# Kernel tuning notes

Measured on AMD Instinct MI355X. Metric: run time of the kernel, lower is better.

The kernel has to match this reference:

```python
import jax, jax.numpy as jnp
import numpy as np

N, IN_C, OUT_C, FEAT_C, G = 1_000_000, 64, 64, 128, 4096


def setup_inputs() -> dict:
    key = jax.random.key(0)
    ks = jax.random.split(key, 9)
    x = jax.random.normal(ks[0], (N, IN_C), dtype=jnp.float32)
    origin_feat = jax.random.normal(ks[1], (G, FEAT_C), dtype=jnp.float32)
    latent_point_batch = jax.random.randint(ks[2], (N,), 0, G, dtype=jnp.int32)
    s_fc = 1.0 / np.sqrt(IN_C)
    s_ft = 1.0 / np.sqrt(FEAT_C)
    W_fc = jax.random.uniform(ks[3], (IN_C, OUT_C), jnp.float32, -s_fc, s_fc)
    b_fc = jax.random.uniform(ks[4], (OUT_C,), jnp.float32, -s_fc, s_fc)
    W_mu = jax.random.uniform(ks[5], (FEAT_C, OUT_C), jnp.float32, -s_ft, s_ft)
    b_mu = jax.random.uniform(ks[6], (OUT_C,), jnp.float32, -s_ft, s_ft)
    W_sig = jax.random.uniform(ks[7], (FEAT_C, OUT_C), jnp.float32, -s_ft, s_ft)
    b_sig = jax.random.uniform(ks[8], (OUT_C,), jnp.float32, -s_ft, s_ft)
    return {"x": x, "origin_feat": origin_feat, "latent_point_batch": latent_point_batch,
            "num_groups": G, "W_fc": W_fc, "b_fc": b_fc, "W_mu": W_mu, "b_mu": b_mu,
            "W_sig": W_sig, "b_sig": b_sig}


def _segment_mean(v, seg, num_segments):
    # [N, C] -> [G, C] per-segment mean
    s = jax.ops.segment_sum(v, seg, num_segments=num_segments)
    cnt = jax.ops.segment_sum(jnp.ones((v.shape[0],), v.dtype), seg,
                              num_segments=num_segments)
    return s / jnp.maximum(cnt, 1.0)[:, None]


def reference(x, origin_feat, latent_point_batch, num_groups,
              W_fc, b_fc, W_mu, b_mu, W_sig, b_sig):
    h = x @ W_fc + b_fc                      # [N, outC]
    mu = origin_feat @ W_mu + b_mu           # [G, outC]
    sig = origin_feat @ W_sig + b_sig        # [G, outC]
    seg = latent_point_batch
    h_mean = _segment_mean(h, seg, num_groups)          # [G, outC]
    h_c = h - h_mean[seg]                                # centered
    h_var = _segment_mean(h_c * h_c, seg, num_groups)    # biased var per group
    h_n = h_c / jnp.sqrt(h_var[seg] + 1e-14)
    out = jax.nn.relu(h_n * sig[seg] + mu[seg])
    return out
```

## Files before the change

### kernel.cpp

```cpp
#include <hip/hip_runtime.h>
#include <stdint.h>

#define GMAX 4096
#define NB   256
#define CH   64

__global__ void FCAdaINLayer_68719477052_kernel(int* __restrict__ cnt, int G) {
  int t = blockIdx.x * blockDim.x + threadIdx.x;
  int stride = gridDim.x * blockDim.x;
  for (int i = t; i < G; i += stride) cnt[i] = 0;
}

__global__ __launch_bounds__(256) void k_bhist(const int* __restrict__ lat, int n, int G,
                                               int* __restrict__ hist_b) {
  __shared__ int h[GMAX];
  int b = blockIdx.x, t = threadIdx.x;
  for (int g = t; g < G; g += 256) h[g] = 0;
  __syncthreads();
  int chb = (n + NB - 1) / NB;
  int beg = b * chb, end = min(beg + chb, n);
  for (int i = beg + t; i < end; i += 256) atomicAdd(&h[lat[i]], 1);
  __syncthreads();
  for (int g = t; g < G; g += 256) hist_b[(size_t)b * G + g] = h[g];
}

__global__ void k_scanA(int* __restrict__ hist_b, int G, int* __restrict__ cnt) {
  int g = blockIdx.x * blockDim.x + threadIdx.x;
  if (g >= G) return;
  int run = 0;
  for (int b = 0; b < NB; b++) {
    int v = hist_b[(size_t)b * G + g];
    hist_b[(size_t)b * G + g] = run;
    run += v;
  }
  cnt[g] = run;
}

__global__ void k_scanB(const int* __restrict__ cnt, int G, int* __restrict__ offs) {
  __shared__ int part[256];
  int t = threadIdx.x;
  int per = (G + 255) / 256;
  int base = t * per;
  int s = 0;
  for (int j = 0; j < per; j++) { int g = base + j; if (g < G) s += cnt[g]; }
  part[t] = s;
  __syncthreads();
  if (t == 0) {
    int run = 0;
    for (int j = 0; j < 256; j++) { int v = part[j]; part[j] = run; run += v; }
  }
  __syncthreads();
  int run = part[t];
  for (int j = 0; j < per; j++) {
    int g = base + j;
    if (g < G) { offs[g] = run; run += cnt[g]; }
  }
  if (t == 255) offs[G] = run;
}

__global__ __launch_bounds__(256) void k_scatter2(const int* __restrict__ lat, int n, int G,
                                                  const int* __restrict__ offs,
                                                  const int* __restrict__ hist_b,
                                                  int* __restrict__ sorted) {
  __shared__ int cur[GMAX];
  int b = blockIdx.x, t = threadIdx.x;
  for (int g = t; g < G; g += 256) cur[g] = offs[g] + hist_b[(size_t)b * G + g];
  __syncthreads();
  int chb = (n + NB - 1) / NB;
  int beg = b * chb, end = min(beg + chb, n);
  for (int i = beg + t; i < end; i += 256) {
    int g = lat[i];
    int pos = atomicAdd(&cur[g], 1);
    sorted[pos] = i;
  }
}

__device__ __forceinline__ float dot64(const float4* __restrict__ xr,
                                       const float* wcol, float bc) {
  float h0 = bc, h1 = 0.f, h2 = 0.f, h3 = 0.f;
#pragma unroll
  for (int j = 0; j < 16; j++) {
    float4 q = xr[j];
    int k = j * 4;
    h0 = fmaf(q.x, wcol[k], h0);
    h1 = fmaf(q.y, wcol[k + 1], h1);
    h2 = fmaf(q.z, wcol[k + 2], h2);
    h3 = fmaf(q.w, wcol[k + 3], h3);
  }
  return (h0 + h2) + (h1 + h3);
}

__global__ __launch_bounds__(256) void k_stats(
    const float* __restrict__ x, const int* __restrict__ sorted,
    const int* __restrict__ offs, const float* __restrict__ of,
    const float* __restrict__ Wmu, const float* __restrict__ bmu,
    const float* __restrict__ Wsig, const float* __restrict__ bsig,
    const float* __restrict__ Wfc, const float* __restrict__ bfc,
    float* __restrict__ scaleT, float* __restrict__ shiftT) {
  __shared__ float xs[CH * 64];
  __shared__ float red[2][4][64];
  int g = blockIdx.x;
  int beg = offs[g], end = offs[g + 1];
  int cnt = end - beg;
  if (cnt == 0) return;
  int tid = threadIdx.x, lane = tid & 63, wid = tid >> 6;

  float wcol[64];
#pragma unroll
  for (int k = 0; k < 64; k++) wcol[k] = Wfc[k * 64 + lane];
  float bc = bfc[lane];

  float ssum = 0.f, ssq = 0.f;
  for (int c0 = 0; c0 < cnt; c0 += CH) {
    int rows = min(CH, cnt - c0);
    __syncthreads();
    for (int idx = tid; idx < rows * 16; idx += 256) {
      int j = idx >> 4, e = idx & 15;
      int p = sorted[beg + c0 + j];
      reinterpret_cast<float4*>(xs)[j * 16 + e] =
          reinterpret_cast<const float4*>(x + (size_t)p * 64)[e];
    }
    __syncthreads();
    for (int j = wid; j < rows; j += 4) {
      float h = dot64(reinterpret_cast<const float4*>(xs + j * 64), wcol, bc);
      ssum += h;
      ssq = fmaf(h, h, ssq);
    }
  }
  red[0][wid][lane] = ssum;
  red[1][wid][lane] = ssq;
  __syncthreads();
  if (wid == 0) {
    float ts = 0.f, tq = 0.f;
#pragma unroll
    for (int w = 0; w < 4; w++) { ts += red[0][w][lane]; tq += red[1][w][lane]; }
    float inv = 1.0f / (float)cnt;
    float mean = ts * inv;
    float var = fmaxf(tq * inv - mean * mean, 0.f);
    float rstd = rsqrtf(var + 1e-14f);
    const float* ofr = of + (size_t)g * 128;
    float a0 = 0.f, a1 = 0.f;
    for (int k = 0; k < 128; k++) {
      float ov = ofr[k];
      a0 = fmaf(ov, Wmu[k * 64 + lane], a0);
      a1 = fmaf(ov, Wsig[k * 64 + lane], a1);
    }
    float mu = a0 + bmu[lane];
    float sig = a1 + bsig[lane];
    float sc = sig * rstd;
    scaleT[(size_t)g * 64 + lane] = sc;
    shiftT[(size_t)g * 64 + lane] = mu - mean * sc;
  }
}

__global__ __launch_bounds__(256) void k_applyn(
    const float* __restrict__ x, const int* __restrict__ lat, int n,
    const float* __restrict__ scaleT, const float* __restrict__ shiftT,
    const float* __restrict__ Wfc, const float* __restrict__ bfc,
    float* __restrict__ out) {
  __shared__ float xs[CH * 64];
  int tid = threadIdx.x, lane = tid & 63, wid = tid >> 6;
  float wcol[64];
#pragma unroll
  for (int k = 0; k < 64; k++) wcol[k] = Wfc[k * 64 + lane];
  float bc = bfc[lane];

  int nchunks = (n + CH - 1) / CH;
  for (int c = blockIdx.x; c < nchunks; c += gridDim.x) {
    int p0 = c * CH;
    int rows = min(CH, n - p0);
    __syncthreads();
    for (int idx = tid; idx < rows * 16; idx += 256) {
      reinterpret_cast<float4*>(xs)[idx] =
          reinterpret_cast<const float4*>(x + (size_t)p0 * 64)[idx];
    }
    __syncthreads();
    for (int j = wid; j < rows; j += 4) {
      int p = p0 + j;
      int g = lat[p];
      float h = dot64(reinterpret_cast<const float4*>(xs + j * 64), wcol, bc);
      float sc = scaleT[(size_t)g * 64 + lane];
      float sh = shiftT[(size_t)g * 64 + lane];
      out[(size_t)p * 64 + lane] = fmaxf(fmaf(h, sc, sh), 0.f);
    }
  }
}

extern "C" void kernel_launch(void* const* d_in, const int* in_sizes, int n_in,
                              void* d_out, int out_size, void* d_ws, size_t ws_size,
                              hipStream_t stream) {
  const float* x   = (const float*)d_in[0];
  const float* of  = (const float*)d_in[1];
  const int* lat   = (const int*)d_in[2];
  const float* Wfc = (const float*)d_in[4];
  const float* bfc = (const float*)d_in[5];
  const float* Wmu = (const float*)d_in[6];
  const float* bmu = (const float*)d_in[7];
  const float* Wsg = (const float*)d_in[8];
  const float* bsg = (const float*)d_in[9];

  int N = in_sizes[2];
  int G = in_sizes[1] / 128;

  char* ws = (char*)d_ws;
  size_t o = 0;
  int* cnt     = (int*)(ws + o); o += (size_t)G * 4;
  int* offs    = (int*)(ws + o); o += (size_t)(G + 1) * 4;
  o = (o + 255) & ~(size_t)255;
  int* hist_b  = (int*)(ws + o); o += (size_t)NB * G * 4;
  int* sorted  = (int*)(ws + o); o += (size_t)N * 4;
  float* scT   = (float*)(ws + o); o += (size_t)G * 64 * 4;
  float* shT   = (float*)(ws + o); o += (size_t)G * 64 * 4;

  FCAdaINLayer_68719477052_kernel<<<32, 256, 0, stream>>>(cnt, G);
  k_bhist<<<NB, 256, 0, stream>>>(lat, N, G, hist_b);
  k_scanA<<<(G + 255) / 256, 256, 0, stream>>>(hist_b, G, cnt);
  k_scanB<<<1, 256, 0, stream>>>(cnt, G, offs);
  k_scatter2<<<NB, 256, 0, stream>>>(lat, N, G, offs, hist_b, sorted);
  k_stats<<<G, 256, 0, stream>>>(x, sorted, offs, of, Wmu, bmu, Wsg, bsg, Wfc, bfc, scT, shT);
  k_applyn<<<2048, 256, 0, stream>>>(x, lat, N, scT, shT, Wfc, bfc, (float*)d_out);
}
```

Before: 925.1 us.

## Read x rows directly via wave-uniform scalar loads instead of LDS staging

Both the stats and apply kernels stop staging x rows through shared memory with block-wide barriers. Each wave now reads its rows straight from global memory, using readfirstlane so the row address is wave-uniform and the loads can become scalar/broadcast loads, and handles two rows per iteration for more memory-level parallelism. This removes the LDS copy and the __syncthreads overhead, at the cost of relying on the scalar cache path and losing the coalesced bulk loads.

Measured after the change: 1.129 ms. 22.1% more time.

```diff
diff --git a/kernel.cpp b/kernel.cpp
--- a/kernel.cpp
+++ b/kernel.cpp
@@ -3,7 +3,6 @@
 
 #define GMAX 4096
 #define NB   256
-#define CH   64
 
 __global__ void FCAdaINLayer_68719477052_kernel(int* __restrict__ cnt, int G) {
   int t = blockIdx.x * blockDim.x + threadIdx.x;
@@ -97,7 +96,6 @@
     const float* __restrict__ Wsig, const float* __restrict__ bsig,
     const float* __restrict__ Wfc, const float* __restrict__ bfc,
     float* __restrict__ scaleT, float* __restrict__ shiftT) {
-  __shared__ float xs[CH * 64];
   __shared__ float red[2][4][64];
   int g = blockIdx.x;
   int beg = offs[g], end = offs[g + 1];
@@ -111,20 +109,18 @@
   float bc = bfc[lane];
 
   float ssum = 0.f, ssq = 0.f;
-  for (int c0 = 0; c0 < cnt; c0 += CH) {
-    int rows = min(CH, cnt - c0);
-    __syncthreads();
-    for (int idx = tid; idx < rows * 16; idx += 256) {
-      int j = idx >> 4, e = idx & 15;
-      int p = sorted[beg + c0 + j];
-      reinterpret_cast<float4*>(xs)[j * 16 + e] =
-          reinterpret_cast<const float4*>(x + (size_t)p * 64)[e];
-    }
-    __syncthreads();
-    for (int j = wid; j < rows; j += 4) {
-      float h = dot64(reinterpret_cast<const float4*>(xs + j * 64), wcol, bc);
-      ssum += h;
-      ssq = fmaf(h, h, ssq);
+  for (int j = wid; j < cnt; j += 8) {
+    int j2 = j + 4;
+    int p1 = __builtin_amdgcn_readfirstlane(sorted[beg + j]);
+    if (j2 < cnt) {
+      int p2 = __builtin_amdgcn_readfirstlane(sorted[beg + j2]);
+      float h1 = dot64(reinterpret_cast<const float4*>(x + (size_t)p1 * 64), wcol, bc);
+      float h2 = dot64(reinterpret_cast<const float4*>(x + (size_t)p2 * 64), wcol, bc);
+      ssum += h1; ssq = fmaf(h1, h1, ssq);
+      ssum += h2; ssq = fmaf(h2, h2, ssq);
+    } else {
+      float h1 = dot64(reinterpret_cast<const float4*>(x + (size_t)p1 * 64), wcol, bc);
+      ssum += h1; ssq = fmaf(h1, h1, ssq);
     }
   }
   red[0][wid][lane] = ssum;
@@ -158,30 +154,34 @@
     const float* __restrict__ scaleT, const float* __restrict__ shiftT,
     const float* __restrict__ Wfc, const float* __restrict__ bfc,
     float* __restrict__ out) {
-  __shared__ float xs[CH * 64];
   int tid = threadIdx.x, lane = tid & 63, wid = tid >> 6;
   float wcol[64];
 #pragma unroll
   for (int k = 0; k < 64; k++) wcol[k] = Wfc[k * 64 + lane];
   float bc = bfc[lane];
 
-  int nchunks = (n + CH - 1) / CH;
-  for (int c = blockIdx.x; c < nchunks; c += gridDim.x) {
-    int p0 = c * CH;
-    int rows = min(CH, n - p0);
-    __syncthreads();
-    for (int idx = tid; idx < rows * 16; idx += 256) {
-      reinterpret_cast<float4*>(xs)[idx] =
-          reinterpret_cast<const float4*>(x + (size_t)p0 * 64)[idx];
-    }
-    __syncthreads();
-    for (int j = wid; j < rows; j += 4) {
-      int p = p0 + j;
-      int g = lat[p];
-      float h = dot64(reinterpret_cast<const float4*>(xs + j * 64), wcol, bc);
-      float sc = scaleT[(size_t)g * 64 + lane];
-      float sh = shiftT[(size_t)g * 64 + lane];
-      out[(size_t)p * 64 + lane] = fmaxf(fmaf(h, sc, sh), 0.f);
+  int nw = gridDim.x * 4;
+  int gw = blockIdx.x * 4 + wid;
+  for (int p0 = gw; p0 < n; p0 += 2 * nw) {
+    int q2 = p0 + nw;
+    int p1 = __builtin_amdgcn_readfirstlane(p0);
+    if (q2 < n) {
+      int p2 = __builtin_amdgcn_readfirstlane(q2);
+      float h1 = dot64(reinterpret_cast<const float4*>(x + (size_t)p1 * 64), wcol, bc);
+      float h2 = dot64(reinterpret_cast<const float4*>(x + (size_t)p2 * 64), wcol, bc);
+      int g1 = lat[p1], g2 = lat[p2];
+      float sc1 = scaleT[(size_t)g1 * 64 + lane];
+      float sh1 = shiftT[(size_t)g1 * 64 + lane];
+      float sc2 = scaleT[(size_t)g2 * 64 + lane];
+      float sh2 = shiftT[(size_t)g2 * 64 + lane];
+      out[(size_t)p1 * 64 + lane] = fmaxf(fmaf(h1, sc1, sh1), 0.f);
+      out[(size_t)p2 * 64 + lane] = fmaxf(fmaf(h2, sc2, sh2), 0.f);
+    } else {
+      float h1 = dot64(reinterpret_cast<const float4*>(x + (size_t)p1 * 64), wcol, bc);
+      int g1 = lat[p1];
+      float sc1 = scaleT[(size_t)g1 * 64 + lane];
+      float sh1 = shiftT[(size_t)g1 * 64 + lane];
+      out[(size_t)p1 * 64 + lane] = fmaxf(fmaf(h1, sc1, sh1), 0.f);
     }
   }
 }
```
